# Performance work log

Measured on AMD Instinct MI355X. Metric: run time of the kernel, lower is better.

## Reference

```python
import jax, jax.numpy as jnp
import numpy as np

B, T, D, H, L = 64, 512, 1024, 1024, 4


def setup_inputs() -> dict:
    key = jax.random.key(0)
    ks = jax.random.split(key, 7)
    s = 1.0 / np.sqrt(H)
    x = jax.random.normal(ks[0], (B, T, D), dtype=jnp.float32)
    dt = jax.random.uniform(ks[1], (B, T), dtype=jnp.float32)  # positive time deltas
    W_ih = jax.random.uniform(ks[2], (L, 3 * H, D), minval=-s, maxval=s, dtype=jnp.float32)
    W_hh = jax.random.uniform(ks[3], (L, 3 * H, H), minval=-s, maxval=s, dtype=jnp.float32)
    b_ih = jax.random.uniform(ks[4], (L, 3 * H), minval=-s, maxval=s, dtype=jnp.float32)
    b_hh = jax.random.uniform(ks[5], (L, 3 * H), minval=-s, maxval=s, dtype=jnp.float32)
    tau = jax.random.uniform(ks[6], (L, H), minval=0.5, maxval=2.0, dtype=jnp.float32)
    return {"x": x, "dt": dt, "W_ih": W_ih, "W_hh": W_hh, "b_ih": b_ih, "b_hh": b_hh, "tau": tau}


def reference(x, dt, W_ih, W_hh, b_ih, b_hh, tau):
    # x: [B,T,D], dt: [B,T]; stacked per-layer params: W_ih [L,3H,D], W_hh [L,3H,H],
    # b_ih/b_hh [L,3H], tau [L,H] (learned time constants, 'exp' scaling).
    n_layers = W_hh.shape[0]
    hid = W_hh.shape[2]
    inv_tau = 1.0 / jax.nn.softplus(tau)  # [L,H]

    def step(h, xt):
        # h: [B,L,H]; x_t: [B,D]; dt_t: [B]
        x_t, dt_t = xt
        inp = x_t
        new_h = []
        for i in range(n_layers):  # fixed small layer count
            decay = jnp.exp(-dt_t[:, None] * inv_tau[i])        # [B,H] exp time scaling
            hd = h[:, i] * decay
            gx = inp @ W_ih[i].T + b_ih[i]                       # [B,3H]
            gh = hd @ W_hh[i].T + b_hh[i]                        # [B,3H]
            xr, xz, xn = jnp.split(gx, 3, axis=-1)
            hr, hz, hn = jnp.split(gh, 3, axis=-1)
            r = jax.nn.sigmoid(xr + hr)
            z = jax.nn.sigmoid(xz + hz)
            n = jnp.tanh(xn + r * hn)
            h_i = (1.0 - z) * n + z * hd                         # torch GRU convention
            new_h.append(h_i)
            inp = h_i
        return jnp.stack(new_h, axis=1), new_h[-1]

    h0 = jnp.zeros((x.shape[0], n_layers, hid), dtype=x.dtype)
    xs = (jnp.swapaxes(x, 0, 1), jnp.swapaxes(dt, 0, 1))  # time-major for scan
    _, seq = jax.lax.scan(step, h0, xs)                    # seq: [T,B,H]
    return jnp.swapaxes(seq, 0, 1)                         # [B,T,H]
```

## Files before the change

kernel.cpp:

```cpp
#include <hip/hip_runtime.h>

typedef _Float16 f16;
typedef _Float16 half8 __attribute__((ext_vector_type(8)));
typedef float f32x4 __attribute__((ext_vector_type(4)));
typedef float f32x2 __attribute__((ext_vector_type(2)));

#define TT 512
#define HID 1024

__device__ __forceinline__ half8 cvt8(f32x4 lo, f32x4 hi) {
  half8 r;
  r[0]=(f16)lo[0]; r[1]=(f16)lo[1]; r[2]=(f16)lo[2]; r[3]=(f16)lo[3];
  r[4]=(f16)hi[0]; r[5]=(f16)hi[1]; r[6]=(f16)hi[2]; r[7]=(f16)hi[3];
  return r;
}
__device__ __forceinline__ void st_sc_u32(unsigned* p, unsigned v) {
  asm volatile("global_store_dword %0, %1, off sc0 sc1" :: "v"(p), "v"(v) : "memory");
}
__device__ __forceinline__ unsigned ld_sc_u32(const unsigned* p) {
  unsigned v;
  asm volatile("global_load_dword %0, %1, off sc0 sc1\n\ts_waitcnt vmcnt(0)"
               : "=v"(v) : "v"(p) : "memory");
  return v;
}
__device__ __forceinline__ void pollPadded(const unsigned* base) {
  const unsigned* p = base + (size_t)(threadIdx.x & 63)*32;
  int gd = 0;
  while (__ballot(ld_sc_u32(p) == 0u)) {
    __builtin_amdgcn_s_sleep(1);
    if (++gd > (1<<20)) break;
  }
}
__device__ __forceinline__ void semSet(int* p, int v) {
  __hip_atomic_store(p, v, __ATOMIC_RELEASE, __HIP_MEMORY_SCOPE_WORKGROUP);
}
__device__ __forceinline__ void semWait(int* p, int v) {
  int gd = 0;
  while (__hip_atomic_load(p, __ATOMIC_ACQUIRE, __HIP_MEMORY_SCOPE_WORKGROUP) < v) {
    if (++gd > (1<<22)) break;
  }
}
__device__ __forceinline__ float sigm(float x)  { return 1.f/(1.f + __expf(-x)); }
__device__ __forceinline__ float ftanh(float x) { return 1.f - 2.f/(1.f + __expf(2.f*x)); }

__global__ void init_misc(const float* __restrict__ x, f16* __restrict__ xh) {
  size_t idx = (size_t)blockIdx.x*256 + threadIdx.x;
  size_t i = idx*8;
  int d = (int)(i & 1023);
  size_t bt = i >> 10;
  int t = (int)(bt & 511), b = (int)(bt >> 9);
  f32x4 a = *(const f32x4*)(x+i);
  f32x4 c4 = *(const f32x4*)(x+i+4);
  int s = d >> 4, c = d & 15;
  *(half8*)(xh + (((size_t)t*64 + s)*64 + b)*16 + c) = cvt8(a,c4);
}

__global__ __launch_bounds__(512, 2) void tsgru_k(
    const float* __restrict__ dtp, const float* __restrict__ Wih,
    const float* __restrict__ Whh, const float* __restrict__ bih,
    const float* __restrict__ bhh, const float* __restrict__ tau,
    const f16* __restrict__ xh, f16* __restrict__ H, f16* __restrict__ HD,
    unsigned* __restrict__ flags, float* __restrict__ out) {
  extern __shared__ char lds[];
  float* PART  = (float*)lds;
  float* biasS = (float*)(lds + 104448);
  int*   sem   = (int*)(lds + 104832);

  const int tid = threadIdx.x, lane = tid & 63, wv = tid >> 6;
  const int g = wv >> 2, kc = wv & 3;
  const int bid = blockIdx.x;
  const int layer = (bid & 7) >> 1;
  const int wgl = (bid >> 3) | ((bid & 1) << 5);
  const int col0 = wgl * 16;
  const int u = (lane >> 4) & 3;

  const float* WL = (g ? Whh : Wih) + (size_t)layer*3072*HID;
  const int wcol = col0 + (lane & 15);
  half8 bW[3][8];
  #pragma unroll
  for (int q=0;q<3;q++)
    #pragma unroll
    for (int ks=0;ks<8;ks++) {
      const float* p = WL + (size_t)(q*HID + wcol)*HID + kc*256 + ks*32 + u*8;
      bW[q][ks] = cvt8(*(const f32x4*)p, *(const f32x4*)(p+4));
    }

  if (tid < 96) {
    int j = tid >> 4, c = tid & 15;
    biasS[tid] = (j < 3) ? bih[layer*3072 + j*HID + col0 + c]
                         : bhh[layer*3072 + (j-3)*HID + col0 + c];
  }
  if (tid < 2) sem[tid] = 0;
  const int gb = tid >> 3, gc2 = (tid & 7)*2;
  const float ni0 = -1.f/log1pf(expf(tau[layer*HID + col0 + gc2]));
  const float ni1 = -1.f/log1pf(expf(tau[layer*HID + col0 + gc2 + 1]));
  __syncthreads();

  const int baseA = (kc*16 + (u>>1))*1024 + (lane&15)*16 + (u&1)*8;
  const f16* gxBase = (layer==0) ? xh : H + (size_t)(layer-1)*TT*65536;
  f16* HDl = HD + (size_t)layer*32*65536;
  unsigned* flagOwn = flags + (size_t)layer*TT*64*32;
  const unsigned* flagUp = flags + (size_t)(layer>0 ? layer-1 : 0)*TT*64*32;

  float hdv0 = 0.f, hdv1 = 0.f;

  for (int t = 0; t < TT; ++t) {
    const float dtg1 = (t < TT-1) ? dtp[gb*TT + t + 1] : 0.f;

    f32x4 acc[4][3];
    #pragma unroll
    for (int m=0;m<4;m++) { acc[m][0]=(f32x4){0.f,0.f,0.f,0.f}; acc[m][1]=acc[m][0]; acc[m][2]=acc[m][0]; }

    if (g == 0) {
      if (wv == 0) {
        if (layer > 0) pollPadded(flagUp + (size_t)t*64*32);
        semSet(sem, t+1);
      } else {
        semWait(sem, t+1);
      }
      const f16* P = gxBase + (size_t)t*65536;
      half8 aF[3][4];
      #pragma unroll
      for (int c=0;c<3;c++)
        #pragma unroll
        for (int m=0;m<4;m++)
          aF[c][m] = *(const half8*)(P + baseA + c*2048 + m*256);
      #pragma unroll
      for (int ks=0;ks<8;ks++) {
        #pragma unroll
        for (int m=0;m<4;m++) {
          const half8 a = aF[ks%3][m];
          acc[m][0] = __builtin_amdgcn_mfma_f32_16x16x32_f16(a, bW[0][ks], acc[m][0],0,0,0);
          acc[m][1] = __builtin_amdgcn_mfma_f32_16x16x32_f16(a, bW[1][ks], acc[m][1],0,0,0);
          acc[m][2] = __builtin_amdgcn_mfma_f32_16x16x32_f16(a, bW[2][ks], acc[m][2],0,0,0);
        }
        if (ks < 5) {
          #pragma unroll
          for (int m=0;m<4;m++)
            aF[(ks+3)%3][m] = *(const half8*)(P + baseA + (ks+3)*2048 + m*256);
        }
      }
    } else {
      if (wv == 4) {
        if (t > 0) pollPadded(flagOwn + (size_t)(t-1)*64*32);
        semSet(sem+1, t+1);
      } else {
        semWait(sem+1, t+1);
      }
      if (t > 0) {
        const f16* P = HDl + (size_t)(t & 31)*65536;
        half8 aF[3][4];
        #pragma unroll
        for (int c=0;c<3;c++)
          #pragma unroll
          for (int m=0;m<4;m++)
            aF[c][m] = *(const half8*)(P + baseA + c*2048 + m*256);
        #pragma unroll
        for (int ks=0;ks<8;ks++) {
          #pragma unroll
          for (int m=0;m<4;m++) {
            const half8 a = aF[ks%3][m];
            acc[m][0] = __builtin_amdgcn_mfma_f32_16x16x32_f16(a, bW[0][ks], acc[m][0],0,0,0);
            acc[m][1] = __builtin_amdgcn_mfma_f32_16x16x32_f16(a, bW[1][ks], acc[m][1],0,0,0);
            acc[m][2] = __builtin_amdgcn_mfma_f32_16x16x32_f16(a, bW[2][ks], acc[m][2],0,0,0);
          }
          if (ks < 5) {
            #pragma unroll
            for (int m=0;m<4;m++)
              aF[(ks+3)%3][m] = *(const half8*)(P + baseA + (ks+3)*2048 + m*256);
          }
        }
      }
    }

    {
      float* Pb = PART + (size_t)(wv*3)*1088 + (lane&15)*68 + u*4;
      #pragma unroll
      for (int q=0;q<3;q++)
        #pragma unroll
        for (int m=0;m<4;m++)
          *(f32x4*)(Pb + q*1088 + m*16) = acc[m][q];
    }
    asm volatile("s_waitcnt lgkmcnt(0)" ::: "memory");
    __builtin_amdgcn_s_barrier();

    {
      float hv[2];
      #pragma unroll
      for (int e=0;e<2;e++) {
        const int pb = (gc2+e)*68 + gb;
        float SX0=0.f,SX1=0.f,SX2=0.f,SH0=0.f,SH1=0.f,SH2=0.f;
        #pragma unroll
        for (int w=0;w<4;w++) {
          const float* Px = PART + (size_t)(w*3)*1088 + pb;
          SX0 += Px[0]; SX1 += Px[1088]; SX2 += Px[2176];
          const float* Ph = PART + (size_t)((4+w)*3)*1088 + pb;
          SH0 += Ph[0]; SH1 += Ph[1088]; SH2 += Ph[2176];
        }
        const float hdv = e ? hdv1 : hdv0;
        const float r = sigm(SX0 + biasS[gc2+e]    + SH0 + biasS[48+gc2+e]);
        const float z = sigm(SX1 + biasS[16+gc2+e] + SH1 + biasS[64+gc2+e]);
        const float n = ftanh(SX2 + biasS[32+gc2+e] + r*(SH2 + biasS[80+gc2+e]));
        hv[e] = (1.f - z)*n + z*hdv;
      }
      union { f16 h[2]; unsigned uu; } pk;
      const size_t slot = (size_t)(wgl*64 + gb)*16 + gc2;
      if (layer < 3) {
        pk.h[0]=(f16)hv[0]; pk.h[1]=(f16)hv[1];
        st_sc_u32((unsigned*)(H + ((size_t)layer*TT + t)*65536 + slot), pk.uu);
      } else {
        f32x2 v; v[0]=hv[0]; v[1]=hv[1];
        *(f32x2*)(out + ((size_t)gb*TT + t)*HID + col0 + gc2) = v;
      }
      if (t < TT-1) {
        hdv0 = hv[0]*__expf(dtg1*ni0);
        hdv1 = hv[1]*__expf(dtg1*ni1);
        pk.h[0]=(f16)hdv0; pk.h[1]=(f16)hdv1;
        st_sc_u32((unsigned*)(HDl + (size_t)((t+1)&31)*65536 + slot), pk.uu);
      }
    }
    asm volatile("s_waitcnt vmcnt(0)" ::: "memory");
    __builtin_amdgcn_s_barrier();
    if (tid == 0) st_sc_u32(flagOwn + ((size_t)t*64 + wgl)*32, 1u);
  }
}

extern "C" void kernel_launch(void* const* d_in, const int* in_sizes, int n_in,
                              void* d_out, int out_size, void* d_ws, size_t ws_size,
                              hipStream_t stream) {
  const float* x   = (const float*)d_in[0];
  const float* dtp = (const float*)d_in[1];
  const float* Wih = (const float*)d_in[2];
  const float* Whh = (const float*)d_in[3];
  const float* bih = (const float*)d_in[4];
  const float* bhh = (const float*)d_in[5];
  const float* tau = (const float*)d_in[6];
  float* out = (float*)d_out;
  char* ws = (char*)d_ws;

  f16* xh = (f16*)ws;
  f16* H  = (f16*)(ws + 67108864);
  f16* HD = (f16*)(ws + 268435456);
  unsigned* flags = (unsigned*)(ws + 285212672);

  (void)hipMemsetAsync(flags, 0, 16777216, stream);
  init_misc<<<16384, 256, 0, stream>>>(x, xh);
  const int ldsBytes = 104960;
  (void)hipFuncSetAttribute((const void*)tsgru_k, hipFuncAttributeMaxDynamicSharedMemorySize, ldsBytes);
  tsgru_k<<<256, 512, ldsBytes, stream>>>(dtp, Wih, Whh, bih, bhh, tau, xh, H, HD, flags, out);
}
```

Baseline: 4.520 ms.

## Embed version keys in hidden-state cells and defer gate math into next step

Replaces the per-step flag poll for the recurrent hidden state with self-validating 16-byte cells that carry a version key next to the fp16 data. Consumers spin on the data itself, chunk by chunk, so they no longer need a separate flag round trip. The gate computation for step t-1 moves into the input-GEMM waves at the start of step t, which overlaps it with the other group's recurrent loads and drops one barrier and the intra-workgroup semaphores. Biases are folded into registers. The cost is doubled HD storage for the key padding, an extra memset, and more complex polling that could spin or misread if the key protocol is wrong.

```diff
diff --git a/kernel.cpp b/kernel.cpp
--- a/kernel.cpp
+++ b/kernel.cpp
@@ -3,10 +3,12 @@
 typedef _Float16 f16;
 typedef _Float16 half8 __attribute__((ext_vector_type(8)));
 typedef float f32x4 __attribute__((ext_vector_type(4)));
-typedef float f32x2 __attribute__((ext_vector_type(2)));
+typedef unsigned u32x4 __attribute__((ext_vector_type(4)));
+typedef unsigned u32x2 __attribute__((ext_vector_type(2)));
 
 #define TT 512
 #define HID 1024
+#define VKEY 0x5AD00000u
 
 __device__ __forceinline__ half8 cvt8(f32x4 lo, f32x4 hi) {
   half8 r;
@@ -14,31 +16,25 @@
   r[4]=(f16)hi[0]; r[5]=(f16)hi[1]; r[6]=(f16)hi[2]; r[7]=(f16)hi[3];
   return r;
 }
-__device__ __forceinline__ void st_sc_u32(unsigned* p, unsigned v) {
+__device__ __forceinline__ void st_sc32(unsigned* p, unsigned v) {
   asm volatile("global_store_dword %0, %1, off sc0 sc1" :: "v"(p), "v"(v) : "memory");
 }
-__device__ __forceinline__ unsigned ld_sc_u32(const unsigned* p) {
+__device__ __forceinline__ void st_sc64(void* p, u32x2 v) {
+  asm volatile("global_store_dwordx2 %0, %1, off sc0 sc1" :: "v"(p), "v"(v) : "memory");
+}
+__device__ __forceinline__ void st_sc128(void* p, u32x4 v) {
+  asm volatile("global_store_dwordx4 %0, %1, off sc0 sc1" :: "v"(p), "v"(v) : "memory");
+}
+__device__ __forceinline__ unsigned ld_sc32(const unsigned* p) {
   unsigned v;
-  asm volatile("global_load_dword %0, %1, off sc0 sc1\n\ts_waitcnt vmcnt(0)"
+  asm volatile("global_load_dword %0, %1, off sc0 sc1\ns_waitcnt vmcnt(0)"
                : "=v"(v) : "v"(p) : "memory");
   return v;
 }
-__device__ __forceinline__ void pollPadded(const unsigned* base) {
-  const unsigned* p = base + (size_t)(threadIdx.x & 63)*32;
-  int gd = 0;
-  while (__ballot(ld_sc_u32(p) == 0u)) {
-    __builtin_amdgcn_s_sleep(1);
-    if (++gd > (1<<20)) break;
-  }
-}
-__device__ __forceinline__ void semSet(int* p, int v) {
-  __hip_atomic_store(p, v, __ATOMIC_RELEASE, __HIP_MEMORY_SCOPE_WORKGROUP);
-}
-__device__ __forceinline__ void semWait(int* p, int v) {
-  int gd = 0;
-  while (__hip_atomic_load(p, __ATOMIC_ACQUIRE, __HIP_MEMORY_SCOPE_WORKGROUP) < v) {
-    if (++gd > (1<<22)) break;
-  }
+__device__ __forceinline__ u32x4 ld_sc128_nw(const u32x4* p) {
+  u32x4 v;
+  asm volatile("global_load_dwordx4 %0, %1, off sc0 sc1" : "=v"(v) : "v"(p) : "memory");
+  return v;
 }
 __device__ __forceinline__ float sigm(float x)  { return 1.f/(1.f + __expf(-x)); }
 __device__ __forceinline__ float ftanh(float x) { return 1.f - 2.f/(1.f + __expf(2.f*x)); }
@@ -59,64 +55,101 @@
     const float* __restrict__ dtp, const float* __restrict__ Wih,
     const float* __restrict__ Whh, const float* __restrict__ bih,
     const float* __restrict__ bhh, const float* __restrict__ tau,
-    const f16* __restrict__ xh, f16* __restrict__ H, f16* __restrict__ HD,
-    unsigned* __restrict__ flags, float* __restrict__ out) {
+    const f16* __restrict__ xh, f16* __restrict__ H,
+    u32x4* __restrict__ HDV, unsigned* __restrict__ fDown,
+    float* __restrict__ out) {
   extern __shared__ char lds[];
-  float* PART  = (float*)lds;
-  float* biasS = (float*)(lds + 104448);
-  int*   sem   = (int*)(lds + 104832);
+  float* PART = (float*)lds;
 
   const int tid = threadIdx.x, lane = tid & 63, wv = tid >> 6;
-  const int g = wv >> 2, kc = wv & 3;
+  const int g = wv >> 2, kh = wv & 3;
   const int bid = blockIdx.x;
   const int layer = (bid & 7) >> 1;
   const int wgl = (bid >> 3) | ((bid & 1) << 5);
   const int col0 = wgl * 16;
-  const int u = (lane >> 4) & 3;
+  const int rA = lane & 15, uA = lane >> 4;
 
   const float* WL = (g ? Whh : Wih) + (size_t)layer*3072*HID;
-  const int wcol = col0 + (lane & 15);
+  const int wcol = col0 + rA;
   half8 bW[3][8];
   #pragma unroll
   for (int q=0;q<3;q++)
     #pragma unroll
     for (int ks=0;ks<8;ks++) {
-      const float* p = WL + (size_t)(q*HID + wcol)*HID + kc*256 + ks*32 + u*8;
+      const float* p = WL + (size_t)(q*HID + wcol)*HID + kh*256 + ks*32 + uA*8;
       bW[q][ks] = cvt8(*(const f32x4*)p, *(const f32x4*)(p+4));
     }
 
-  if (tid < 96) {
-    int j = tid >> 4, c = tid & 15;
-    biasS[tid] = (j < 3) ? bih[layer*3072 + j*HID + col0 + c]
-                         : bhh[layer*3072 + (j-3)*HID + col0 + c];
+  const int gb = tid >> 2, cg4 = (tid & 3) * 4;
+  float bbR[4],bbZ[4],biN4[4],bhN4[4],ni[4],hdv[4];
+  if (tid < 256) {
+    #pragma unroll
+    for (int e=0;e<4;e++) {
+      const int col = col0 + cg4 + e;
+      bbR[e]  = bih[layer*3072 + col]        + bhh[layer*3072 + col];
+      bbZ[e]  = bih[layer*3072 + 1024 + col] + bhh[layer*3072 + 1024 + col];
+      biN4[e] = bih[layer*3072 + 2048 + col];
+      bhN4[e] = bhh[layer*3072 + 2048 + col];
+      ni[e]   = -1.f/log1pf(expf(tau[layer*HID + col]));
+      hdv[e]  = 0.f;
+    }
   }
-  if (tid < 2) sem[tid] = 0;
-  const int gb = tid >> 3, gc2 = (tid & 7)*2;
-  const float ni0 = -1.f/log1pf(expf(tau[layer*HID + col0 + gc2]));
-  const float ni1 = -1.f/log1pf(expf(tau[layer*HID + col0 + gc2 + 1]));
-  __syncthreads();
-
-  const int baseA = (kc*16 + (u>>1))*1024 + (lane&15)*16 + (u&1)*8;
+
+  const int baseA = (kh*16 + (uA>>1))*1024 + rA*16 + (uA&1)*8;
+  const int cb = baseA >> 2;
   const f16* gxBase = (layer==0) ? xh : H + (size_t)(layer-1)*TT*65536;
-  f16* HDl = HD + (size_t)layer*32*65536;
-  unsigned* flagOwn = flags + (size_t)layer*TT*64*32;
-  const unsigned* flagUp = flags + (size_t)(layer>0 ? layer-1 : 0)*TT*64*32;
-
-  float hdv0 = 0.f, hdv1 = 0.f;
+  u32x4* HDVl = HDV + (size_t)layer*32*16384;
+
+  auto doGate = [&](int tg, bool storeHd) {
+    const float dtg = (tg < TT-1) ? dtp[gb*TT + tg + 1] : 0.f;
+    float hv[4];
+    #pragma unroll
+    for (int e=0;e<4;e++) {
+      const int pb = (cg4+e)*68 + gb;
+      float SX0=0.f,SX1=0.f,SX2=0.f,SH0=0.f,SH1=0.f,SH2=0.f;
+      #pragma unroll
+      for (int w=0;w<4;w++) {
+        const float* Px = PART + (size_t)(w*3)*1088 + pb;
+        SX0 += Px[0]; SX1 += Px[1088]; SX2 += Px[2176];
+        const float* Ph = PART + (size_t)((4+w)*3)*1088 + pb;
+        SH0 += Ph[0]; SH1 += Ph[1088]; SH2 += Ph[2176];
+      }
+      const float r = sigm(SX0 + SH0 + bbR[e]);
+      const float z = sigm(SX1 + SH1 + bbZ[e]);
+      const float n = ftanh(SX2 + biN4[e] + r*(SH2 + bhN4[e]));
+      hv[e] = (1.f - z)*n + z*hdv[e];
+      hdv[e] = hv[e] * __expf(dtg * ni[e]);
+    }
+    if (layer < 3) {
+      union { f16 h[4]; u32x2 u; } ph;
+      #pragma unroll
+      for (int e=0;e<4;e++) ph.h[e] = (f16)hv[e];
+      st_sc64(H + ((size_t)layer*TT + tg)*65536 + (size_t)(wgl*64+gb)*16 + cg4, ph.u);
+    } else {
+      f32x4 ov; ov[0]=hv[0]; ov[1]=hv[1]; ov[2]=hv[2]; ov[3]=hv[3];
+      *(f32x4*)(out + ((size_t)gb*TT + tg)*HID + col0 + cg4) = ov;
+    }
+    if (storeHd && tg < TT-1) {
+      union { f16 h[4]; u32x2 u; } pd;
+      #pragma unroll
+      for (int e=0;e<4;e++) pd.h[e] = (f16)hdv[e];
+      u32x4 cell; cell[0]=pd.u[0]; cell[1]=pd.u[1];
+      cell[2] = VKEY | (unsigned)(tg+1); cell[3] = 0u;
+      st_sc128(HDVl + (size_t)((tg+1)&31)*16384 + (size_t)(wgl*64+gb)*4 + (tid&3), cell);
+    }
+  };
 
   for (int t = 0; t < TT; ++t) {
-    const float dtg1 = (t < TT-1) ? dtp[gb*TT + t + 1] : 0.f;
-
     f32x4 acc[4][3];
     #pragma unroll
     for (int m=0;m<4;m++) { acc[m][0]=(f32x4){0.f,0.f,0.f,0.f}; acc[m][1]=acc[m][0]; acc[m][2]=acc[m][0]; }
 
     if (g == 0) {
-      if (wv == 0) {
-        if (layer > 0) pollPadded(flagUp + (size_t)t*64*32);
-        semSet(sem, t+1);
-      } else {
-        semWait(sem, t+1);
+      if (t > 0 && tid < 256) doGate(t-1, true);
+      if (layer > 0) {
+        const unsigned* fp = fDown + (((size_t)(layer-1)*TT + t)*64 + lane)*32;
+        int gd = 0;
+        while (__ballot(ld_sc32(fp) == 0u)) { __builtin_amdgcn_s_sleep(2); if (++gd > (1<<20)) break; }
       }
       const f16* P = gxBase + (size_t)t*65536;
       half8 aF[3][4];
@@ -140,41 +173,60 @@
             aF[(ks+3)%3][m] = *(const half8*)(P + baseA + (ks+3)*2048 + m*256);
         }
       }
-    } else {
-      if (wv == 4) {
-        if (t > 0) pollPadded(flagOwn + (size_t)(t-1)*64*32);
-        semSet(sem+1, t+1);
-      } else {
-        semWait(sem+1, t+1);
-      }
-      if (t > 0) {
-        const f16* P = HDl + (size_t)(t & 31)*65536;
-        half8 aF[3][4];
-        #pragma unroll
-        for (int c=0;c<3;c++)
+      asm volatile("s_waitcnt vmcnt(0)" ::: "memory");
+    } else if (t > 0) {
+      const u32x4* Pc = HDVl + (size_t)(t & 31)*16384;
+      const unsigned key = VKEY | (unsigned)t;
+      u32x4 cw[2][4][2];
+      #pragma unroll
+      for (int par=0;par<2;par++)
+        #pragma unroll
+        for (int m=0;m<4;m++) {
+          cw[par][m][0] = Pc[cb + par*512 + m*64];
+          cw[par][m][1] = Pc[cb + par*512 + m*64 + 1];
+        }
+      #pragma unroll
+      for (int ks=0;ks<8;ks++) {
+        const int par = ks & 1;
+        int gd = 0;
+        for (;;) {
+          bool ok = true;
           #pragma unroll
           for (int m=0;m<4;m++)
-            aF[c][m] = *(const half8*)(P + baseA + c*2048 + m*256);
-        #pragma unroll
-        for (int ks=0;ks<8;ks++) {
+            ok = ok && (cw[par][m][0][2] == key) && (cw[par][m][1][2] == key);
+          if (__ballot(!ok) == 0ull) break;
           #pragma unroll
           for (int m=0;m<4;m++) {
-            const half8 a = aF[ks%3][m];
-            acc[m][0] = __builtin_amdgcn_mfma_f32_16x16x32_f16(a, bW[0][ks], acc[m][0],0,0,0);
-            acc[m][1] = __builtin_amdgcn_mfma_f32_16x16x32_f16(a, bW[1][ks], acc[m][1],0,0,0);
-            acc[m][2] = __builtin_amdgcn_mfma_f32_16x16x32_f16(a, bW[2][ks], acc[m][2],0,0,0);
+            cw[par][m][0] = ld_sc128_nw(&Pc[cb + ks*512 + m*64]);
+            cw[par][m][1] = ld_sc128_nw(&Pc[cb + ks*512 + m*64 + 1]);
           }
-          if (ks < 5) {
-            #pragma unroll
-            for (int m=0;m<4;m++)
-              aF[(ks+3)%3][m] = *(const half8*)(P + baseA + (ks+3)*2048 + m*256);
+          asm volatile("s_waitcnt vmcnt(0)" ::: "memory");
+          __builtin_amdgcn_sched_barrier(0);
+          __builtin_amdgcn_s_sleep(1);
+          if (++gd > (1<<19)) break;
+        }
+        #pragma unroll
+        for (int m=0;m<4;m++) {
+          union { unsigned w[4]; half8 h; } av;
+          av.w[0]=cw[par][m][0][0]; av.w[1]=cw[par][m][0][1];
+          av.w[2]=cw[par][m][1][0]; av.w[3]=cw[par][m][1][1];
+          acc[m][0] = __builtin_amdgcn_mfma_f32_16x16x32_f16(av.h, bW[0][ks], acc[m][0],0,0,0);
+          acc[m][1] = __builtin_amdgcn_mfma_f32_16x16x32_f16(av.h, bW[1][ks], acc[m][1],0,0,0);
+          acc[m][2] = __builtin_amdgcn_mfma_f32_16x16x32_f16(av.h, bW[2][ks], acc[m][2],0,0,0);
+        }
+        if (ks < 6) {
+          #pragma unroll
+          for (int m=0;m<4;m++) {
+            cw[par][m][0] = Pc[cb + (ks+2)*512 + m*64];
+            cw[par][m][1] = Pc[cb + (ks+2)*512 + m*64 + 1];
           }
         }
       }
     }
 
+    __builtin_amdgcn_s_barrier();
     {
-      float* Pb = PART + (size_t)(wv*3)*1088 + (lane&15)*68 + u*4;
+      float* Pb = PART + (size_t)(wv*3)*1088 + rA*68 + uA*4;
       #pragma unroll
       for (int q=0;q<3;q++)
         #pragma unroll
@@ -183,46 +235,15 @@
     }
     asm volatile("s_waitcnt lgkmcnt(0)" ::: "memory");
     __builtin_amdgcn_s_barrier();
-
-    {
-      float hv[2];
-      #pragma unroll
-      for (int e=0;e<2;e++) {
-        const int pb = (gc2+e)*68 + gb;
-        float SX0=0.f,SX1=0.f,SX2=0.f,SH0=0.f,SH1=0.f,SH2=0.f;
-        #pragma unroll
-        for (int w=0;w<4;w++) {
-          const float* Px = PART + (size_t)(w*3)*1088 + pb;
-          SX0 += Px[0]; SX1 += Px[1088]; SX2 += Px[2176];
-          const float* Ph = PART + (size_t)((4+w)*3)*1088 + pb;
-          SH0 += Ph[0]; SH1 += Ph[1088]; SH2 += Ph[2176];
-        }
-        const float hdv = e ? hdv1 : hdv0;
-        const float r = sigm(SX0 + biasS[gc2+e]    + SH0 + biasS[48+gc2+e]);
-        const float z = sigm(SX1 + biasS[16+gc2+e] + SH1 + biasS[64+gc2+e]);
-        const float n = ftanh(SX2 + biasS[32+gc2+e] + r*(SH2 + biasS[80+gc2+e]));
-        hv[e] = (1.f - z)*n + z*hdv;
-      }
-      union { f16 h[2]; unsigned uu; } pk;
-      const size_t slot = (size_t)(wgl*64 + gb)*16 + gc2;
-      if (layer < 3) {
-        pk.h[0]=(f16)hv[0]; pk.h[1]=(f16)hv[1];
-        st_sc_u32((unsigned*)(H + ((size_t)layer*TT + t)*65536 + slot), pk.uu);
-      } else {
-        f32x2 v; v[0]=hv[0]; v[1]=hv[1];
-        *(f32x2*)(out + ((size_t)gb*TT + t)*HID + col0 + gc2) = v;
-      }
-      if (t < TT-1) {
-        hdv0 = hv[0]*__expf(dtg1*ni0);
-        hdv1 = hv[1]*__expf(dtg1*ni1);
-        pk.h[0]=(f16)hdv0; pk.h[1]=(f16)hdv1;
-        st_sc_u32((unsigned*)(HDl + (size_t)((t+1)&31)*65536 + slot), pk.uu);
-      }
-    }
-    asm volatile("s_waitcnt vmcnt(0)" ::: "memory");
-    __builtin_amdgcn_s_barrier();
-    if (tid == 0) st_sc_u32(flagOwn + ((size_t)t*64 + wgl)*32, 1u);
+    if (tid == 0 && t > 0 && layer < 3)
+      st_sc32(fDown + (((size_t)layer*TT + (t-1))*64 + wgl)*32, 1u);
   }
+
+  if (tid < 256) doGate(TT-1, false);
+  asm volatile("s_waitcnt vmcnt(0)" ::: "memory");
+  __builtin_amdgcn_s_barrier();
+  if (tid == 0 && layer < 3)
+    st_sc32(fDown + (((size_t)layer*TT + (TT-1))*64 + wgl)*32, 1u);
 }
 
 extern "C" void kernel_launch(void* const* d_in, const int* in_sizes, int n_in,
@@ -240,12 +261,13 @@
 
   f16* xh = (f16*)ws;
   f16* H  = (f16*)(ws + 67108864);
-  f16* HD = (f16*)(ws + 268435456);
-  unsigned* flags = (unsigned*)(ws + 285212672);
-
-  (void)hipMemsetAsync(flags, 0, 16777216, stream);
+  u32x4* HDV = (u32x4*)(ws + 268435456);
+  unsigned* fDown = (unsigned*)(ws + 268435456 + 33554432);
+
+  (void)hipMemsetAsync(HDV, 0, 33554432, stream);
+  (void)hipMemsetAsync(fDown, 0, 16777216, stream);
   init_misc<<<16384, 256, 0, stream>>>(x, xh);
-  const int ldsBytes = 104960;
+  const int ldsBytes = 104448;
   (void)hipFuncSetAttribute((const void*)tsgru_k, hipFuncAttributeMaxDynamicSharedMemorySize, ldsBytes);
-  tsgru_k<<<256, 512, ldsBytes, stream>>>(dtp, Wih, Whh, bih, bhh, tau, xh, H, HD, flags, out);
-}
+  tsgru_k<<<256, 512, ldsBytes, stream>>>(dtp, Wih, Whh, bih, bhh, tau, xh, H, HDV, fDown, out);
+}
```

Result: slower. 8.152 ms (+80.4%).
